# Performance work log

Measured on AMD Instinct MI355X. Metric: run time of the kernel, lower is better.

Reference implementation:

```python
import jax, jax.numpy as jnp
import numpy as np

N0, N1, E, B = 100000, 100000, 800000, 1024
F0, F1 = 93, 43


def _gin(x, src, dst, w, b, n):
    # GINConv(eps=0): h_i = Lin(x_i + sum_{j->i} x_j)
    agg = jax.ops.segment_sum(x[src], dst, num_segments=n)
    return (x + agg) @ w + b


def _pool(x, batch, num_graphs):
    s = jax.ops.segment_sum(x, batch, num_segments=num_graphs)
    cnt = jax.ops.segment_sum(jnp.ones((x.shape[0],), x.dtype), batch, num_segments=num_graphs)
    mean = s / jnp.maximum(cnt, 1.0)[:, None]
    mx = jax.ops.segment_max(x, batch, num_segments=num_graphs)
    return jnp.concatenate([mean, mx], axis=1)


def _pairnorm(x, eps=1e-5):
    x = x - x.mean(axis=0, keepdims=True)
    return x / jnp.sqrt(eps + (x * x).sum(-1).mean())


def _bn(x, gamma, beta, eps=1e-5):
    mu = x.mean(axis=0, keepdims=True)
    var = x.var(axis=0, keepdims=True)
    return (x - mu) / jnp.sqrt(var + eps) * gamma + beta


def _branch(x, ei, batch, n, wc_a, bc_a, wc_b, bc_b, fg_w1, fg_b1, fg_w2, fg_b2, fg_g, fg_bt, ff_w1, ff_b1, ff_w2, ff_b2):
    src, dst = ei[0], ei[1]
    h = jax.nn.relu(_gin(x, src, dst, wc_a, bc_a, n))
    h = jax.nn.relu(_gin(h, src, dst, wc_b, bc_b, n))
    g = _pairnorm(_pool(h, batch, B))
    g = jax.nn.relu(g @ fg_w1 + fg_b1)
    g = _bn(g @ fg_w2 + fg_b2, fg_g, fg_bt)  # [B, 512]
    z = jax.nn.relu(g @ ff_w1 + ff_b1)
    z = jax.nn.sigmoid(z @ ff_w2 + ff_b2)  # [B, 2]
    return z[:, 0], z[:, 1], g


def setup_inputs() -> dict:
    key = jax.random.key(0)
    ks = iter(jax.random.split(key, 40))

    def lin(fan_in, fan_out):
        bnd = 1.0 / np.sqrt(fan_in)
        w = jax.random.uniform(next(ks), (fan_in, fan_out), jnp.float32, -bnd, bnd)
        b = jax.random.uniform(next(ks), (fan_out,), jnp.float32, -bnd, bnd)
        return w, b

    x0 = jax.random.normal(next(ks), (N0, F0), jnp.float32)
    x1 = jax.random.normal(next(ks), (N1, F1), jnp.float32)
    ei0 = jax.random.randint(next(ks), (2, E), 0, N0, jnp.int32)
    ei1 = jax.random.randint(next(ks), (2, E), 0, N1, jnp.int32)
    b0 = jnp.sort(jax.random.randint(next(ks), (N0,), 0, B, jnp.int32))
    b1 = jnp.sort(jax.random.randint(next(ks), (N1,), 0, B, jnp.int32))

    inp = {"x0": x0, "edge_index_0": ei0, "batch_0": b0, "x1": x1, "edge_index_1": ei1, "batch_1": b1}
    inp["w_c1"], inp["b_c1"] = lin(F0, F0)
    inp["w_c2"], inp["b_c2"] = lin(F0, F0 * 10)
    inp["w_c3"], inp["b_c3"] = lin(F1, F1)
    inp["w_c4"], inp["b_c4"] = lin(F1, F1 * 10)
    inp["fg0_w1"], inp["fg0_b1"] = lin(F0 * 10 * 2, 1024)
    inp["fg0_w2"], inp["fg0_b2"] = lin(1024, 512)
    inp["fg0_g"], inp["fg0_bt"] = jnp.ones((512,), jnp.float32), jnp.zeros((512,), jnp.float32)
    inp["fg1_w1"], inp["fg1_b1"] = lin(F1 * 10 * 2, 1024)
    inp["fg1_w2"], inp["fg1_b2"] = lin(1024, 512)
    inp["fg1_g"], inp["fg1_bt"] = jnp.ones((512,), jnp.float32), jnp.zeros((512,), jnp.float32)
    inp["ff0_w1"], inp["ff0_b1"] = lin(512, 256)
    inp["ff0_w2"], inp["ff0_b2"] = lin(256, 2)
    inp["ff1_w1"], inp["ff1_b1"] = lin(512, 256)
    inp["ff1_w2"], inp["ff1_b2"] = lin(256, 2)
    return inp


def reference(x0, edge_index_0, batch_0, x1, edge_index_1, batch_1,
              w_c1, b_c1, w_c2, b_c2, w_c3, b_c3, w_c4, b_c4,
              fg0_w1, fg0_b1, fg0_w2, fg0_b2, fg0_g, fg0_bt,
              fg1_w1, fg1_b1, fg1_w2, fg1_b2, fg1_g, fg1_bt,
              ff0_w1, ff0_b1, ff0_w2, ff0_b2,
              ff1_w1, ff1_b1, ff1_w2, ff1_b2):
    alpha, beta, xg0 = _branch(x0, edge_index_0, batch_0, N0, w_c1, b_c1, w_c2, b_c2,
                               fg0_w1, fg0_b1, fg0_w2, fg0_b2, fg0_g, fg0_bt,
                               ff0_w1, ff0_b1, ff0_w2, ff0_b2)
    alpha1, beta1, xg1 = _branch(x1, edge_index_1, batch_1, N1, w_c3, b_c3, w_c4, b_c4,
                                 fg1_w1, fg1_b1, fg1_w2, fg1_b2, fg1_g, fg1_bt,
                                 ff1_w1, ff1_b1, ff1_w2, ff1_b2)
    return (alpha, beta, xg0, xg1, alpha1, beta1)
```

## Files before the change

kernel.cpp:

```cpp
#include <hip/hip_runtime.h>
#include <hip/hip_bf16.h>
#include <math.h>

#define EDGES 800000
#define NNODES 100000
#define NGRAPH 1024
#define SCAN_B 256

typedef __attribute__((ext_vector_type(8))) short short8v;
typedef __attribute__((ext_vector_type(4))) float float4v;
typedef unsigned short ushort_t;

__device__ inline ushort_t f2bf(float f) {
  __hip_bfloat16 h = __float2bfloat16(f);
  return *reinterpret_cast<ushort_t*>(&h);
}
__device__ inline float bf2f(ushort_t u) {
  return __uint_as_float(((unsigned int)u) << 16);
}

__global__ __launch_bounds__(256) void deg_k(const int* __restrict__ dst,
                                             int* __restrict__ deg, int E) {
  int e = blockIdx.x * 256 + threadIdx.x;
  if (e < E) atomicAdd(&deg[dst[e]], 1);
}

__global__ __launch_bounds__(SCAN_B) void scan_block_k(const int* __restrict__ deg,
                                                       int* __restrict__ scanned,
                                                       int* __restrict__ bsum, int n) {
  __shared__ int tmp[SCAN_B];
  int b = blockIdx.x, t = threadIdx.x, i = b * SCAN_B + t;
  int v = (i < n) ? deg[i] : 0;
  tmp[t] = v;
  __syncthreads();
  for (int off = 1; off < SCAN_B; off <<= 1) {
    int x = (t >= off) ? tmp[t - off] : 0;
    __syncthreads();
    tmp[t] += x;
    __syncthreads();
  }
  if (i < n) scanned[i] = tmp[t] - v;
  if (t == SCAN_B - 1) bsum[b] = tmp[t];
}

__global__ __launch_bounds__(512) void scan_sums_k(int* __restrict__ bsum, int nb) {
  __shared__ int tmp[512];
  int t = threadIdx.x;
  int v = (t < nb) ? bsum[t] : 0;
  tmp[t] = v;
  __syncthreads();
  for (int off = 1; off < 512; off <<= 1) {
    int x = (t >= off) ? tmp[t - off] : 0;
    __syncthreads();
    tmp[t] += x;
    __syncthreads();
  }
  if (t < nb) bsum[t] = tmp[t] - v;
}

__global__ __launch_bounds__(256) void scan_add_k(const int* __restrict__ scanned,
                                                  const int* __restrict__ bsum,
                                                  int* __restrict__ rowstart, int n,
                                                  int total) {
  int i = blockIdx.x * 256 + threadIdx.x;
  if (i < n) rowstart[i] = scanned[i] + bsum[i / SCAN_B];
  if (i == 0) rowstart[n] = total;
}

#define NBMAX 512
__global__ __launch_bounds__(256) void bscatter_k(const int* __restrict__ src,
                                                  const int* __restrict__ dst,
                                                  const int* __restrict__ rowstart,
                                                  int* __restrict__ bcur,
                                                  int2* __restrict__ EB, int E,
                                                  int NB) {
  __shared__ int hist[NBMAX], run[NBMAX], lcur[NBMAX];
  int t = threadIdx.x;
  for (int b = t; b < NB; b += 256) {
    hist[b] = 0;
    lcur[b] = 0;
  }
  __syncthreads();
  int e0 = blockIdx.x * 4096;
  int e1 = min(E, e0 + 4096);
  for (int e = e0 + t; e < e1; e += 256) atomicAdd(&hist[dst[e] >> 8], 1);
  __syncthreads();
  for (int b = t; b < NB; b += 256)
    if (hist[b] > 0) run[b] = atomicAdd(&bcur[b], hist[b]);
  __syncthreads();
  for (int e = e0 + t; e < e1; e += 256) {
    int d = dst[e];
    int b = d >> 8;
    int l = atomicAdd(&lcur[b], 1);
    int pos = rowstart[b << 8] + run[b] + l;
    EB[pos] = make_int2(src[e], d);
  }
}

__global__ __launch_bounds__(256) void fill2_k(const int2* __restrict__ EB,
                                               const int* __restrict__ rowstart,
                                               int* __restrict__ cur,
                                               int* __restrict__ adj, int E) {
  int e = blockIdx.x * 256 + threadIdx.x;
  if (e >= E) return;
  int2 ed = EB[e];
  int p = rowstart[ed.y] + atomicAdd(&cur[ed.y], 1);
  adj[p] = ed.x;
}

__global__ __launch_bounds__(256) void gstart_k(const int* __restrict__ bat,
                                                int* __restrict__ gs, int N, int B) {
  int g = blockIdx.x * 256 + threadIdx.x;
  if (g > B) return;
  if (g == B) {
    gs[B] = N;
    return;
  }
  int lo = 0, hi = N;
  while (lo < hi) {
    int mid = (lo + hi) >> 1;
    if (bat[mid] < g) lo = mid + 1;
    else hi = mid;
  }
  gs[g] = lo;
}

template <int KP>
__global__ __launch_bounds__(256) void tobf16_k(const float* __restrict__ x,
                                                ushort_t* __restrict__ out, int M,
                                                int F) {
  long i = (long)blockIdx.x * 256 + threadIdx.x;
  if (i >= (long)M * KP) return;
  int r = (int)(i / KP), c = (int)(i % KP);
  float v = (c < F) ? x[(long)r * F + c] : 0.f;
  out[i] = f2bf(v);
}

template <int KP>
__global__ __launch_bounds__(256) void gather_k(const ushort_t* __restrict__ X,
                                                const int* __restrict__ rowstart,
                                                const int* __restrict__ adj,
                                                ushort_t* __restrict__ out, int M) {
  constexpr int CH = KP / 8;
  long tid = (long)blockIdx.x * 256 + threadIdx.x;
  if (tid >= (long)M * CH) return;
  int node = (int)(tid / CH), ch = (int)(tid % CH);
  int o = ch * 8;
  float acc[8];
  uint4 self = *(const uint4*)&X[(long)node * KP + o];
  {
    const unsigned int u[4] = {self.x, self.y, self.z, self.w};
#pragma unroll
    for (int i = 0; i < 4; ++i) {
      acc[2 * i] = __uint_as_float((u[i] & 0xFFFFu) << 16);
      acc[2 * i + 1] = __uint_as_float(u[i] & 0xFFFF0000u);
    }
  }
  int rs = rowstart[node], re = rowstart[node + 1];
  for (int e = rs; e < re; ++e) {
    int j = adj[e];
    uint4 v = *(const uint4*)&X[(long)j * KP + o];
    const unsigned int u[4] = {v.x, v.y, v.z, v.w};
#pragma unroll
    for (int i = 0; i < 4; ++i) {
      acc[2 * i] += __uint_as_float((u[i] & 0xFFFFu) << 16);
      acc[2 * i + 1] += __uint_as_float(u[i] & 0xFFFF0000u);
    }
  }
  uint4 r;
  unsigned int* p = &r.x;
#pragma unroll
  for (int i = 0; i < 4; ++i) {
    unsigned int lo = f2bf(acc[2 * i]);
    unsigned int hi = f2bf(acc[2 * i + 1]);
    p[i] = lo | (hi << 16);
  }
  *(uint4*)&out[(long)node * KP + o] = r;
}

__global__ __launch_bounds__(256) void wt_k(const float* __restrict__ W,
                                            ushort_t* __restrict__ WT, int K, int N,
                                            int KP, int Npad) {
  int i = blockIdx.x * 256 + threadIdx.x;
  if (i >= Npad * KP) return;
  int n = i / KP, k = i % KP;
  float v = (k < K && n < N) ? W[(long)k * N + n] : 0.f;
  WT[i] = f2bf(v);
}

template <int KP>
__global__ __launch_bounds__(256) void conv_gemm2_k(
    const ushort_t* __restrict__ A, const ushort_t* __restrict__ WT,
    const float* __restrict__ bias, ushort_t* __restrict__ Cout, int M, int Nc,
    int OW, int NT) {
  constexpr int NKS = KP / 32;
  int tid = threadIdx.x;
  int wid = tid >> 6, lane = tid & 63;
  int lr = lane & 15, q = lane >> 4;
  int lk = q * 8;
  int row0 = blockIdx.x * 64;
  int arow = row0 + wid * 16 + lr;

  short8v a[NKS];
  const ushort_t* ap = A + (long)arow * KP + lk;
#pragma unroll
  for (int ks = 0; ks < NKS; ++ks) a[ks] = *(const short8v*)(ap + ks * 32);

  for (int ct = 0; ct < NT; ++ct) {
    int col0 = ct * 64;
    float4v acc[4];
#pragma unroll
    for (int i = 0; i < 4; ++i) acc[i] = (float4v){0.f, 0.f, 0.f, 0.f};
#pragma unroll
    for (int ks = 0; ks < NKS; ++ks) {
#pragma unroll
      for (int nf = 0; nf < 4; ++nf) {
        short8v b =
            *(const short8v*)&WT[(long)(col0 + nf * 16 + lr) * KP + ks * 32 + lk];
        acc[nf] = __builtin_amdgcn_mfma_f32_16x16x32_bf16(a[ks], b, acc[nf], 0, 0, 0);
      }
    }
#pragma unroll
    for (int nf = 0; nf < 4; ++nf) {
      int gc = col0 + nf * 16 + lr;
      if (gc >= OW) continue;
      float bv = (gc < Nc) ? bias[gc] : 0.f;
#pragma unroll
      for (int i = 0; i < 4; ++i) {
        int gr = row0 + wid * 16 + q * 4 + i;
        if (gr < M) {
          float v = (gc < Nc) ? fmaxf(acc[nf][i] + bv, 0.f) : 0.f;
          Cout[(long)gr * OW + gc] = f2bf(v);
        }
      }
    }
  }
}

template <int KP>
__global__ __launch_bounds__(64) void conv_pool2_k(
    const ushort_t* __restrict__ A, const ushort_t* __restrict__ WT,
    const float* __restrict__ bias, const int* __restrict__ gstart,
    float* __restrict__ pool, int Nc, int NCpool) {
  constexpr int NKS = KP / 32;
  int g = blockIdx.x;
  int col0 = blockIdx.y * 64;
  int rs = gstart[g], re = gstart[g + 1];
  int rows = re - rs;
  int lane = threadIdx.x;
  int lr = lane & 15, q = lane >> 4, lk = q * 8;

  short8v bfr[NKS][4];
  float bv[4];
#pragma unroll
  for (int nf = 0; nf < 4; ++nf) {
    int gc = col0 + nf * 16 + lr;
    bv[nf] = (gc < Nc) ? bias[gc] : 0.f;
#pragma unroll
    for (int ks = 0; ks < NKS; ++ks)
      bfr[ks][nf] = *(const short8v*)&WT[(long)gc * KP + ks * 32 + lk];
  }

  float wsum[4][4] = {}, wmax[4][4] = {};
  int nch = (rows + 15) / 16;
  for (int c = 0; c < nch; ++c) {
    const ushort_t* ap = A + (long)(rs + c * 16 + lr) * KP + lk;
    short8v a[NKS];
#pragma unroll
    for (int ks = 0; ks < NKS; ++ks) a[ks] = *(const short8v*)(ap + ks * 32);
    float4v acc[4];
#pragma unroll
    for (int i = 0; i < 4; ++i) acc[i] = (float4v){0.f, 0.f, 0.f, 0.f};
#pragma unroll
    for (int ks = 0; ks < NKS; ++ks)
#pragma unroll
      for (int nf = 0; nf < 4; ++nf)
        acc[nf] = __builtin_amdgcn_mfma_f32_16x16x32_bf16(a[ks], bfr[ks][nf],
                                                          acc[nf], 0, 0, 0);
    int rbase = c * 16 + q * 4;
#pragma unroll
    for (int i = 0; i < 4; ++i) {
      bool ok = rbase + i < rows;
#pragma unroll
      for (int nf = 0; nf < 4; ++nf) {
        float v = ok ? fmaxf(acc[nf][i] + bv[nf], 0.f) : 0.f;
        wsum[nf][i] += v;
        wmax[nf][i] = fmaxf(wmax[nf][i], v);
      }
    }
  }

  float inv = 1.f / fmaxf((float)rows, 1.f);
#pragma unroll
  for (int nf = 0; nf < 4; ++nf) {
    float s = (wsum[nf][0] + wsum[nf][1]) + (wsum[nf][2] + wsum[nf][3]);
    float m = fmaxf(fmaxf(wmax[nf][0], wmax[nf][1]),
                    fmaxf(wmax[nf][2], wmax[nf][3]));
    s += __shfl_xor(s, 16);
    s += __shfl_xor(s, 32);
    m = fmaxf(m, __shfl_xor(m, 16));
    m = fmaxf(m, __shfl_xor(m, 32));
    int gc = col0 + nf * 16 + lr;
    if (q == 0 && gc < Nc) {
      pool[(long)g * 2 * NCpool + gc] = s * inv;
      pool[(long)g * 2 * NCpool + NCpool + gc] = m;
    }
  }
}

__global__ __launch_bounds__(256) void fc_mfma_k(const ushort_t* __restrict__ A,
                                                 const ushort_t* __restrict__ WT,
                                                 float* __restrict__ PART, int KP,
                                                 int Nc, int Kc) {
  int tid = threadIdx.x;
  int wid = tid >> 6, lane = tid & 63;
  int lr = lane & 15, q = lane >> 4, lk = q * 8;
  int row0 = blockIdx.y * 64, col0 = blockIdx.x * 64;
  int M = gridDim.y * 64;
  int kbeg = blockIdx.z * Kc;
  int arow = row0 + wid * 16 + lr;
  const ushort_t* ap = A + (long)arow * KP + kbeg + lk;
  const ushort_t* wp = WT + (long)col0 * KP + kbeg + lk;

  float4v acc[4];
#pragma unroll
  for (int i = 0; i < 4; ++i) acc[i] = (float4v){0.f, 0.f, 0.f, 0.f};

  for (int k0 = 0; k0 < Kc; k0 += 32) {
    short8v a = *(const short8v*)(ap + k0);
#pragma unroll
    for (int nf = 0; nf < 4; ++nf) {
      short8v b = *(const short8v*)(wp + (long)(nf * 16 + lr) * KP + k0);
      acc[nf] = __builtin_amdgcn_mfma_f32_16x16x32_bf16(a, b, acc[nf], 0, 0, 0);
    }
  }

  float* P = PART + (long)blockIdx.z * M * Nc;
#pragma unroll
  for (int nf = 0; nf < 4; ++nf) {
    int gc = col0 + nf * 16 + lr;
#pragma unroll
    for (int i = 0; i < 4; ++i) {
      int gr = row0 + wid * 16 + q * 4 + i;
      P[(long)gr * Nc + gc] = acc[nf][i];
    }
  }
}

__global__ __launch_bounds__(256) void sk_epi2_k(const float* __restrict__ PART,
                                                 const float* __restrict__ bias,
                                                 float* __restrict__ Cf,
                                                 ushort_t* __restrict__ Cb, int M,
                                                 int Nc, int SK, int relu) {
  long idx = (long)blockIdx.x * 256 + threadIdx.x;
  if (idx >= (long)M * Nc) return;
  int c = (int)(idx % Nc);
  float s = bias[c];
  for (int z = 0; z < SK; ++z) s += PART[(long)z * M * Nc + idx];
  if (relu) s = fmaxf(s, 0.f);
  if (Cf) Cf[idx] = s;
  if (Cb) Cb[idx] = f2bf(s);
}

__global__ __launch_bounds__(256) void colstat_part_k(const float* __restrict__ X,
                                                      float* __restrict__ PS,
                                                      float* __restrict__ ssqtot,
                                                      int Rows, int Cols, int CR) {
  __shared__ float sred[256];
  int c0 = blockIdx.x * 64;
  int chunk = blockIdx.y;
  int t = threadIdx.x;
  int c = c0 + (t & 63);
  int rg = t >> 6;
  int rbeg = chunk * CR, rend = min(Rows, rbeg + CR);
  float s = 0.f, s2 = 0.f;
  if (c < Cols) {
    for (int r = rbeg + rg; r < rend; r += 4) {
      float v = X[(long)r * Cols + c];
      s += v;
      s2 += v * v;
    }
  }
  sred[t] = s;
  __syncthreads();
  if (t < 64 && c0 + t < Cols)
    PS[(long)chunk * Cols + c0 + t] = sred[t] + sred[t + 64] + sred[t + 128] + sred[t + 192];
  for (int off = 32; off > 0; off >>= 1) s2 += __shfl_down(s2, off);
  if ((t & 63) == 0) atomicAdd(ssqtot, s2);
}

__global__ __launch_bounds__(256) void colstat_fin_k(const float* __restrict__ PS,
                                                     float* __restrict__ cm, int Rows,
                                                     int Cols, int nchunk) {
  int c = blockIdx.x * 256 + threadIdx.x;
  if (c >= Cols) return;
  float s = 0.f;
  for (int z = 0; z < nchunk; ++z) s += PS[(long)z * Cols + c];
  cm[c] = s / Rows;
}

__global__ __launch_bounds__(256) void pn_scale_k(const float* __restrict__ cm,
                                                  const float* __restrict__ ssqtot,
                                                  float* __restrict__ scale, int Rows,
                                                  int Cols) {
  __shared__ float red[256];
  int t = threadIdx.x;
  float s = 0.f;
  for (int i = t; i < Cols; i += 256) {
    float v = cm[i];
    s += v * v;
  }
  red[t] = s;
  __syncthreads();
  for (int off = 128; off > 0; off >>= 1) {
    if (t < off) red[t] += red[t + off];
    __syncthreads();
  }
  if (t == 0) {
    float ssq = ssqtot[0] - (float)Rows * red[0];
    scale[0] = 1.f / sqrtf(1e-5f + ssq / Rows);
  }
}

__global__ __launch_bounds__(256) void pn_apply2_k(const float* __restrict__ X,
                                                   const float* __restrict__ cm,
                                                   const float* __restrict__ scale,
                                                   ushort_t* __restrict__ outB,
                                                   int Rows, int Cols, int KP1) {
  long idx = (long)blockIdx.x * 256 + threadIdx.x;
  if (idx >= (long)Rows * KP1) return;
  int r = (int)(idx / KP1), c = (int)(idx % KP1);
  float v = 0.f;
  if (c < Cols) v = (X[(long)r * Cols + c] - cm[c]) * scale[0];
  outB[idx] = f2bf(v);
}

__global__ __launch_bounds__(256) void bn_part_k(const float* __restrict__ X,
                                                 float* __restrict__ PS,
                                                 float* __restrict__ PQ, int Rows,
                                                 int Cols, int CR) {
  __shared__ float s1[256], s2l[256];
  int c0 = blockIdx.x * 64;
  int chunk = blockIdx.y;
  int t = threadIdx.x;
  int c = c0 + (t & 63);
  int rg = t >> 6;
  int rbeg = chunk * CR, rend = min(Rows, rbeg + CR);
  float a = 0.f, b = 0.f;
  if (c < Cols) {
    for (int r = rbeg + rg; r < rend; r += 4) {
      float v = X[(long)r * Cols + c];
      a += v;
      b += v * v;
    }
  }
  s1[t] = a;
  s2l[t] = b;
  __syncthreads();
  if (t < 64 && c0 + t < Cols) {
    PS[(long)chunk * Cols + c0 + t] = s1[t] + s1[t + 64] + s1[t + 128] + s1[t + 192];
    PQ[(long)chunk * Cols + c0 + t] = s2l[t] + s2l[t + 64] + s2l[t + 128] + s2l[t + 192];
  }
}

__global__ __launch_bounds__(256) void bn_fin_k(const float* __restrict__ PS,
                                                const float* __restrict__ PQ,
                                                float* __restrict__ mu,
                                                float* __restrict__ var, int Rows,
                                                int Cols, int nchunk) {
  int c = blockIdx.x * 256 + threadIdx.x;
  if (c >= Cols) return;
  float s = 0.f, q = 0.f;
  for (int z = 0; z < nchunk; ++z) {
    s += PS[(long)z * Cols + c];
    q += PQ[(long)z * Cols + c];
  }
  float m = s / Rows;
  mu[c] = m;
  var[c] = q / Rows - m * m;
}

__global__ void bn_apply2_k(float* __restrict__ X, const float* __restrict__ mu,
                            const float* __restrict__ var, const float* __restrict__ g,
                            const float* __restrict__ b, ushort_t* __restrict__ XB16,
                            int Rows, int Cols) {
  long idx = (long)blockIdx.x * 256 + threadIdx.x;
  if (idx >= (long)Rows * Cols) return;
  int c = (int)(idx % Cols);
  float v = (X[idx] - mu[c]) / sqrtf(var[c] + 1e-5f) * g[c] + b[c];
  X[idx] = v;
  XB16[idx] = f2bf(v);
}

__global__ __launch_bounds__(64) void ff2_k(const ushort_t* __restrict__ Z,
                                            const float* __restrict__ W2,
                                            const float* __restrict__ b2,
                                            float* __restrict__ alpha,
                                            float* __restrict__ beta, int K) {
  int row = blockIdx.x;
  int t = threadIdx.x;
  float s0 = 0.f, s1 = 0.f;
  for (int k = t; k < K; k += 64) {
    float z = bf2f(Z[(long)row * K + k]);
    s0 += z * W2[2 * k];
    s1 += z * W2[2 * k + 1];
  }
  for (int off = 32; off > 0; off >>= 1) {
    s0 += __shfl_down(s0, off);
    s1 += __shfl_down(s1, off);
  }
  if (t == 0) {
    alpha[row] = 1.f / (1.f + expf(-(s0 + b2[0])));
    beta[row] = 1.f / (1.f + expf(-(s1 + b2[1])));
  }
}

template <int KP>
static void run_branch(const float* x, const int* ei, const int* bat,
                       const float* wc1, const float* bc1, const float* wc2,
                       const float* bc2, const float* fgw1, const float* fgb1,
                       const float* fgw2, const float* fgb2, const float* fgg,
                       const float* fgbt, const float* ffw1, const float* ffb1,
                       const float* ffw2, const float* ffb2, int N, int F,
                       float* out_alpha, float* out_beta, float* out_xg,
                       ushort_t* XB, ushort_t* XA, ushort_t* H, ushort_t* WT,
                       int* deg, int* scanned, int* rowstart, int* cur, int* bsum,
                       int* bcur, int* adj, int* GS, float* POOL, float* CM,
                       float* MU, float* VAR, float* SSQ, float* PSUM, float* PSQ,
                       ushort_t* POOLB, ushort_t* WTF1, ushort_t* WTF2,
                       ushort_t* WTFF, ushort_t* G1B, ushort_t* XGB, ushort_t* Z1B,
                       float* PART, hipStream_t stream) {
  const int NC = F * 10;
  const int Bn = NGRAPH;
  const int* src = ei;
  const int* dst = ei + EDGES;
  const int MB = (N + 63) / 64;
  const int Mpad = MB * 64;
  const int nb = (N + SCAN_B - 1) / SCAN_B;
  const int NB = (N + 255) >> 8;

  int2* EB = (int2*)XB;
  hipMemsetAsync(deg, 0, (size_t)N * 4, stream);
  hipMemsetAsync(cur, 0, (size_t)N * 4, stream);
  hipMemsetAsync(bcur, 0, NBMAX * 4, stream);
  deg_k<<<(EDGES + 255) / 256, 256, 0, stream>>>(dst, deg, EDGES);
  scan_block_k<<<nb, SCAN_B, 0, stream>>>(deg, scanned, bsum, N);
  scan_sums_k<<<1, 512, 0, stream>>>(bsum, nb);
  scan_add_k<<<nb, 256, 0, stream>>>(scanned, bsum, rowstart, N, EDGES);
  bscatter_k<<<(EDGES + 4095) / 4096, 256, 0, stream>>>(src, dst, rowstart, bcur, EB, EDGES, NB);
  fill2_k<<<(EDGES + 255) / 256, 256, 0, stream>>>(EB, rowstart, cur, adj, EDGES);
  gstart_k<<<(NGRAPH + 256) / 256, 256, 0, stream>>>(bat, GS, N, NGRAPH);

  constexpr int CH = KP / 8;
  if (Mpad > N)
    hipMemsetAsync(XA + (size_t)N * KP, 0, (size_t)(Mpad - N) * KP * 2, stream);
  tobf16_k<KP><<<(int)(((long)N * KP + 255) / 256), 256, 0, stream>>>(x, XB, N, F);
  gather_k<KP><<<(int)(((long)N * CH + 255) / 256), 256, 0, stream>>>(XB, rowstart, adj, XA, N);
  wt_k<<<(((F + 63) / 64) * 64 * KP + 255) / 256, 256, 0, stream>>>(
      wc1, WT, F, F, KP, ((F + 63) / 64) * 64);
  conv_gemm2_k<KP><<<MB, 256, 0, stream>>>(XA, WT, bc1, H, N, F, KP, (KP + 63) / 64);
  gather_k<KP><<<(int)(((long)N * CH + 255) / 256), 256, 0, stream>>>(H, rowstart, adj, XA, N);
  int Npad2 = ((NC + 63) / 64) * 64;
  wt_k<<<(Npad2 * KP + 255) / 256, 256, 0, stream>>>(wc2, WT, F, NC, KP, Npad2);
  conv_pool2_k<KP><<<dim3(NGRAPH, Npad2 / 64), 64, 0, stream>>>(XA, WT, bc2, GS, POOL, NC, NC);

  int Cols = 2 * NC;
  const int NCH = 16, CR = NGRAPH / NCH;
  hipMemsetAsync(SSQ, 0, 8, stream);
  colstat_part_k<<<dim3((Cols + 63) / 64, NCH), 256, 0, stream>>>(POOL, PSUM, SSQ, Bn, Cols, CR);
  colstat_fin_k<<<(Cols + 255) / 256, 256, 0, stream>>>(PSUM, CM, Bn, Cols, NCH);
  pn_scale_k<<<1, 256, 0, stream>>>(CM, SSQ, SSQ + 1, Bn, Cols);

  int KP1 = ((Cols + 127) / 128) * 128;
  pn_apply2_k<<<(int)(((long)Bn * KP1 + 255) / 256), 256, 0, stream>>>(
      POOL, CM, SSQ + 1, POOLB, Bn, Cols, KP1);
  wt_k<<<(1024 * KP1 + 255) / 256, 256, 0, stream>>>(fgw1, WTF1, Cols, 1024, KP1, 1024);
  fc_mfma_k<<<dim3(16, 16, 4), 256, 0, stream>>>(POOLB, WTF1, PART, KP1, 1024, KP1 / 4);
  sk_epi2_k<<<(Bn * 1024 + 255) / 256, 256, 0, stream>>>(PART, fgb1, nullptr, G1B, Bn, 1024, 4, 1);
  wt_k<<<(512 * 1024 + 255) / 256, 256, 0, stream>>>(fgw2, WTF2, 1024, 512, 1024, 512);
  fc_mfma_k<<<dim3(8, 16, 4), 256, 0, stream>>>(G1B, WTF2, PART, 1024, 512, 256);
  sk_epi2_k<<<(Bn * 512 + 255) / 256, 256, 0, stream>>>(PART, fgb2, out_xg, nullptr, Bn, 512, 4, 0);
  bn_part_k<<<dim3(8, 8), 256, 0, stream>>>(out_xg, PSUM, PSQ, Bn, 512, 128);
  bn_fin_k<<<2, 256, 0, stream>>>(PSUM, PSQ, MU, VAR, Bn, 512, 8);
  bn_apply2_k<<<(Bn * 512 + 255) / 256, 256, 0, stream>>>(out_xg, MU, VAR, fgg, fgbt, XGB, Bn, 512);
  wt_k<<<(256 * 512 + 255) / 256, 256, 0, stream>>>(ffw1, WTFF, 512, 256, 512, 256);
  fc_mfma_k<<<dim3(4, 16, 8), 256, 0, stream>>>(XGB, WTFF, PART, 512, 256, 64);
  sk_epi2_k<<<(Bn * 256 + 255) / 256, 256, 0, stream>>>(PART, ffb1, nullptr, Z1B, Bn, 256, 8, 1);
  ff2_k<<<Bn, 64, 0, stream>>>(Z1B, ffw2, ffb2, out_alpha, out_beta, 256);
}

extern "C" void kernel_launch(void* const* d_in, const int* in_sizes, int n_in,
                              void* d_out, int out_size, void* d_ws, size_t ws_size,
                              hipStream_t stream) {
  if (n_in < 34) return;
  const float* x0 = (const float*)d_in[0];
  const int* ei0 = (const int*)d_in[1];
  const int* b0 = (const int*)d_in[2];
  const float* x1 = (const float*)d_in[3];
  const int* ei1 = (const int*)d_in[4];
  const int* b1 = (const int*)d_in[5];
  const float* w_c1 = (const float*)d_in[6];
  const float* b_c1 = (const float*)d_in[7];
  const float* w_c2 = (const float*)d_in[8];
  const float* b_c2 = (const float*)d_in[9];
  const float* w_c3 = (const float*)d_in[10];
  const float* b_c3 = (const float*)d_in[11];
  const float* w_c4 = (const float*)d_in[12];
  const float* b_c4 = (const float*)d_in[13];
  const float* fg0_w1 = (const float*)d_in[14];
  const float* fg0_b1 = (const float*)d_in[15];
  const float* fg0_w2 = (const float*)d_in[16];
  const float* fg0_b2 = (const float*)d_in[17];
  const float* fg0_g = (const float*)d_in[18];
  const float* fg0_bt = (const float*)d_in[19];
  const float* fg1_w1 = (const float*)d_in[20];
  const float* fg1_b1 = (const float*)d_in[21];
  const float* fg1_w2 = (const float*)d_in[22];
  const float* fg1_b2 = (const float*)d_in[23];
  const float* fg1_g = (const float*)d_in[24];
  const float* fg1_bt = (const float*)d_in[25];
  const float* ff0_w1 = (const float*)d_in[26];
  const float* ff0_b1 = (const float*)d_in[27];
  const float* ff0_w2 = (const float*)d_in[28];
  const float* ff0_b2 = (const float*)d_in[29];
  const float* ff1_w1 = (const float*)d_in[30];
  const float* ff1_b1 = (const float*)d_in[31];
  const float* ff1_w2 = (const float*)d_in[32];
  const float* ff1_b2 = (const float*)d_in[33];

  float* out = (float*)d_out;
  float* alpha = out;
  float* beta = out + 1024;
  float* xg0 = out + 2048;
  float* xg1 = out + 2048 + 1024 * 512;
  float* alpha1 = out + 2048 + 2 * 1024 * 512;
  float* beta1 = alpha1 + 1024;

  char* w = (char*)d_ws;
  auto alloc = [&](size_t bytes) -> void* {
    void* p = (void*)w;
    w += ((bytes + 255) / 256) * 256;
    return p;
  };
  const int Mpad = ((NNODES + 63) / 64) * 64;
  ushort_t* XB = (ushort_t*)alloc((size_t)Mpad * 96 * 2);
  ushort_t* XA = (ushort_t*)alloc((size_t)Mpad * 96 * 2);
  ushort_t* H = (ushort_t*)alloc((size_t)Mpad * 96 * 2);
  ushort_t* WT = (ushort_t*)alloc((size_t)960 * 96 * 2);
  int* deg = (int*)alloc((size_t)(NNODES + 1) * 4);
  int* scanned = (int*)alloc((size_t)(NNODES + 1) * 4);
  int* rowstart = (int*)alloc((size_t)(NNODES + 1) * 4);
  int* cur = (int*)alloc((size_t)NNODES * 4);
  int* bsum = (int*)alloc(512 * 4);
  int* bcur = (int*)alloc(NBMAX * 4);
  int* adj = (int*)alloc((size_t)EDGES * 4);
  int* GS = (int*)alloc((size_t)(NGRAPH + 1) * 4);
  float* POOL = (float*)alloc((size_t)NGRAPH * 1860 * 4);
  float* CM = (float*)alloc(1860 * 4);
  float* MU = (float*)alloc(512 * 4);
  float* VAR = (float*)alloc(512 * 4);
  float* SSQ = (float*)alloc(256);
  float* PSUM = (float*)alloc((size_t)16 * 1920 * 4);
  float* PSQ = (float*)alloc((size_t)8 * 512 * 4);
  ushort_t* POOLB = (ushort_t*)alloc((size_t)NGRAPH * 1920 * 2);
  ushort_t* WTF1 = (ushort_t*)alloc((size_t)1024 * 1920 * 2);
  ushort_t* WTF2 = (ushort_t*)alloc((size_t)512 * 1024 * 2);
  ushort_t* WTFF = (ushort_t*)alloc((size_t)256 * 512 * 2);
  ushort_t* G1B = (ushort_t*)alloc((size_t)NGRAPH * 1024 * 2);
  ushort_t* XGB = (ushort_t*)alloc((size_t)NGRAPH * 512 * 2);
  ushort_t* Z1B = (ushort_t*)alloc((size_t)NGRAPH * 256 * 2);
  if ((size_t)(w - (char*)d_ws) > ws_size) return;

  float* PART = (float*)XB;

  run_branch<96>(x0, ei0, b0, w_c1, b_c1, w_c2, b_c2, fg0_w1, fg0_b1, fg0_w2,
                 fg0_b2, fg0_g, fg0_bt, ff0_w1, ff0_b1, ff0_w2, ff0_b2, NNODES,
                 93, alpha, beta, xg0, XB, XA, H, WT, deg, scanned, rowstart,
                 cur, bsum, bcur, adj, GS, POOL, CM, MU, VAR, SSQ, PSUM, PSQ,
                 POOLB, WTF1, WTF2, WTFF, G1B, XGB, Z1B, PART, stream);
  run_branch<64>(x1, ei1, b1, w_c3, b_c3, w_c4, b_c4, fg1_w1, fg1_b1, fg1_w2,
                 fg1_b2, fg1_g, fg1_bt, ff1_w1, ff1_b1, ff1_w2, ff1_b2, NNODES,
                 43, alpha1, beta1, xg1, XB, XA, H, WT, deg, scanned, rowstart,
                 cur, bsum, bcur, adj, GS, POOL, CM, MU, VAR, SSQ, PSUM, PSQ,
                 POOLB, WTF1, WTF2, WTFF, G1B, XGB, Z1B, PART, stream);
}
```

Measured before the change: 720.1 us.

## Build CSR via two-level bucket sort instead of per-node degree scan

Replaces the per-node degree atomics, three-kernel multi-block scan and global-atomic CSR fill with a bucket-level count and scan over 256-node buckets. A per-bucket kernel then builds node row starts and the adjacency list using shared-memory counting. This removes several launches, two memsets and the global atomics on per-node counters. It adds a shared-memory serial-ish per-bucket pass, whose load depends on bucket size, about 2k edges each.

Result: faster. 629.2 us (-12.6%).

```diff
diff --git a/kernel.cpp b/kernel.cpp
--- a/kernel.cpp
+++ b/kernel.cpp
@@ -5,7 +5,6 @@
 #define EDGES 800000
 #define NNODES 100000
 #define NGRAPH 1024
-#define SCAN_B 256
 
 typedef __attribute__((ext_vector_type(8))) short short8v;
 typedef __attribute__((ext_vector_type(4))) float float4v;
@@ -19,34 +18,28 @@
   return __uint_as_float(((unsigned int)u) << 16);
 }
 
-__global__ __launch_bounds__(256) void deg_k(const int* __restrict__ dst,
-                                             int* __restrict__ deg, int E) {
-  int e = blockIdx.x * 256 + threadIdx.x;
-  if (e < E) atomicAdd(&deg[dst[e]], 1);
-}
-
-__global__ __launch_bounds__(SCAN_B) void scan_block_k(const int* __restrict__ deg,
-                                                       int* __restrict__ scanned,
-                                                       int* __restrict__ bsum, int n) {
-  __shared__ int tmp[SCAN_B];
-  int b = blockIdx.x, t = threadIdx.x, i = b * SCAN_B + t;
-  int v = (i < n) ? deg[i] : 0;
-  tmp[t] = v;
-  __syncthreads();
-  for (int off = 1; off < SCAN_B; off <<= 1) {
-    int x = (t >= off) ? tmp[t - off] : 0;
-    __syncthreads();
-    tmp[t] += x;
-    __syncthreads();
-  }
-  if (i < n) scanned[i] = tmp[t] - v;
-  if (t == SCAN_B - 1) bsum[b] = tmp[t];
-}
-
-__global__ __launch_bounds__(512) void scan_sums_k(int* __restrict__ bsum, int nb) {
+#define NBMAX 512
+
+__global__ __launch_bounds__(256) void bcount_k(const int* __restrict__ dst,
+                                                int* __restrict__ bcnt, int E,
+                                                int NB) {
+  __shared__ int hist[NBMAX];
+  int t = threadIdx.x;
+  for (int b = t; b < NB; b += 256) hist[b] = 0;
+  __syncthreads();
+  int e0 = blockIdx.x * 4096;
+  int e1 = min(E, e0 + 4096);
+  for (int e = e0 + t; e < e1; e += 256) atomicAdd(&hist[dst[e] >> 8], 1);
+  __syncthreads();
+  for (int b = t; b < NB; b += 256)
+    if (hist[b] > 0) atomicAdd(&bcnt[b], hist[b]);
+}
+
+__global__ __launch_bounds__(512) void bscan_k(const int* __restrict__ bcnt,
+                                               int* __restrict__ boff, int NB) {
   __shared__ int tmp[512];
   int t = threadIdx.x;
-  int v = (t < nb) ? bsum[t] : 0;
+  int v = (t < NB) ? bcnt[t] : 0;
   tmp[t] = v;
   __syncthreads();
   for (int off = 1; off < 512; off <<= 1) {
@@ -55,22 +48,13 @@
     tmp[t] += x;
     __syncthreads();
   }
-  if (t < nb) bsum[t] = tmp[t] - v;
-}
-
-__global__ __launch_bounds__(256) void scan_add_k(const int* __restrict__ scanned,
-                                                  const int* __restrict__ bsum,
-                                                  int* __restrict__ rowstart, int n,
-                                                  int total) {
-  int i = blockIdx.x * 256 + threadIdx.x;
-  if (i < n) rowstart[i] = scanned[i] + bsum[i / SCAN_B];
-  if (i == 0) rowstart[n] = total;
-}
-
-#define NBMAX 512
+  if (t < NB) boff[t] = tmp[t] - v;
+  if (t == NB - 1) boff[NB] = tmp[t];
+}
+
 __global__ __launch_bounds__(256) void bscatter_k(const int* __restrict__ src,
                                                   const int* __restrict__ dst,
-                                                  const int* __restrict__ rowstart,
+                                                  const int* __restrict__ boff,
                                                   int* __restrict__ bcur,
                                                   int2* __restrict__ EB, int E,
                                                   int NB) {
@@ -92,20 +76,43 @@
     int d = dst[e];
     int b = d >> 8;
     int l = atomicAdd(&lcur[b], 1);
-    int pos = rowstart[b << 8] + run[b] + l;
+    int pos = boff[b] + run[b] + l;
     EB[pos] = make_int2(src[e], d);
   }
 }
 
-__global__ __launch_bounds__(256) void fill2_k(const int2* __restrict__ EB,
-                                               const int* __restrict__ rowstart,
-                                               int* __restrict__ cur,
-                                               int* __restrict__ adj, int E) {
-  int e = blockIdx.x * 256 + threadIdx.x;
-  if (e >= E) return;
-  int2 ed = EB[e];
-  int p = rowstart[ed.y] + atomicAdd(&cur[ed.y], 1);
-  adj[p] = ed.x;
+__global__ __launch_bounds__(256) void bucket_csr_k(const int2* __restrict__ EB,
+                                                    const int* __restrict__ boff,
+                                                    int* __restrict__ rowstart,
+                                                    int* __restrict__ adj, int N,
+                                                    int NB, int E) {
+  __shared__ int cnt[256], pfx[256], lcur[256];
+  int b = blockIdx.x, t = threadIdx.x;
+  int e0 = boff[b], e1 = boff[b + 1];
+  cnt[t] = 0;
+  __syncthreads();
+  for (int e = e0 + t; e < e1; e += 256) atomicAdd(&cnt[EB[e].y & 255], 1);
+  __syncthreads();
+  int v = cnt[t];
+  pfx[t] = v;
+  __syncthreads();
+  for (int off = 1; off < 256; off <<= 1) {
+    int x = (t >= off) ? pfx[t - off] : 0;
+    __syncthreads();
+    pfx[t] += x;
+    __syncthreads();
+  }
+  int node = (b << 8) + t;
+  if (node < N) rowstart[node] = e0 + pfx[t] - v;
+  if (b == NB - 1 && t == 0) rowstart[N] = E;
+  lcur[t] = 0;
+  __syncthreads();
+  for (int e = e0 + t; e < e1; e += 256) {
+    int2 ed = EB[e];
+    int ln = ed.y & 255;
+    int l = atomicAdd(&lcur[ln], 1);
+    adj[e0 + pfx[ln] - cnt[ln] + l] = ed.x;
+  }
 }
 
 __global__ __launch_bounds__(256) void gstart_k(const int* __restrict__ bat,
@@ -524,31 +531,27 @@
                        const float* ffw2, const float* ffb2, int N, int F,
                        float* out_alpha, float* out_beta, float* out_xg,
                        ushort_t* XB, ushort_t* XA, ushort_t* H, ushort_t* WT,
-                       int* deg, int* scanned, int* rowstart, int* cur, int* bsum,
-                       int* bcur, int* adj, int* GS, float* POOL, float* CM,
-                       float* MU, float* VAR, float* SSQ, float* PSUM, float* PSQ,
-                       ushort_t* POOLB, ushort_t* WTF1, ushort_t* WTF2,
-                       ushort_t* WTFF, ushort_t* G1B, ushort_t* XGB, ushort_t* Z1B,
-                       float* PART, hipStream_t stream) {
+                       int* rowstart, int* BC, int* boff, int* adj, int* GS,
+                       float* POOL, float* CM, float* MU, float* VAR, float* SSQ,
+                       float* PSUM, float* PSQ, ushort_t* POOLB, ushort_t* WTF1,
+                       ushort_t* WTF2, ushort_t* WTFF, ushort_t* G1B, ushort_t* XGB,
+                       ushort_t* Z1B, float* PART, hipStream_t stream) {
   const int NC = F * 10;
   const int Bn = NGRAPH;
   const int* src = ei;
   const int* dst = ei + EDGES;
   const int MB = (N + 63) / 64;
   const int Mpad = MB * 64;
-  const int nb = (N + SCAN_B - 1) / SCAN_B;
   const int NB = (N + 255) >> 8;
 
   int2* EB = (int2*)XB;
-  hipMemsetAsync(deg, 0, (size_t)N * 4, stream);
-  hipMemsetAsync(cur, 0, (size_t)N * 4, stream);
-  hipMemsetAsync(bcur, 0, NBMAX * 4, stream);
-  deg_k<<<(EDGES + 255) / 256, 256, 0, stream>>>(dst, deg, EDGES);
-  scan_block_k<<<nb, SCAN_B, 0, stream>>>(deg, scanned, bsum, N);
-  scan_sums_k<<<1, 512, 0, stream>>>(bsum, nb);
-  scan_add_k<<<nb, 256, 0, stream>>>(scanned, bsum, rowstart, N, EDGES);
-  bscatter_k<<<(EDGES + 4095) / 4096, 256, 0, stream>>>(src, dst, rowstart, bcur, EB, EDGES, NB);
-  fill2_k<<<(EDGES + 255) / 256, 256, 0, stream>>>(EB, rowstart, cur, adj, EDGES);
+  int* bcnt = BC;
+  int* bcur = BC + NBMAX;
+  hipMemsetAsync(BC, 0, 2 * NBMAX * 4, stream);
+  bcount_k<<<(EDGES + 4095) / 4096, 256, 0, stream>>>(dst, bcnt, EDGES, NB);
+  bscan_k<<<1, 512, 0, stream>>>(bcnt, boff, NB);
+  bscatter_k<<<(EDGES + 4095) / 4096, 256, 0, stream>>>(src, dst, boff, bcur, EB, EDGES, NB);
+  bucket_csr_k<<<NB, 256, 0, stream>>>(EB, boff, rowstart, adj, N, NB, EDGES);
   gstart_k<<<(NGRAPH + 256) / 256, 256, 0, stream>>>(bat, GS, N, NGRAPH);
 
   constexpr int CH = KP / 8;
@@ -647,12 +650,9 @@
   ushort_t* XA = (ushort_t*)alloc((size_t)Mpad * 96 * 2);
   ushort_t* H = (ushort_t*)alloc((size_t)Mpad * 96 * 2);
   ushort_t* WT = (ushort_t*)alloc((size_t)960 * 96 * 2);
-  int* deg = (int*)alloc((size_t)(NNODES + 1) * 4);
-  int* scanned = (int*)alloc((size_t)(NNODES + 1) * 4);
   int* rowstart = (int*)alloc((size_t)(NNODES + 1) * 4);
-  int* cur = (int*)alloc((size_t)NNODES * 4);
-  int* bsum = (int*)alloc(512 * 4);
-  int* bcur = (int*)alloc(NBMAX * 4);
+  int* BC = (int*)alloc(2 * NBMAX * 4);
+  int* boff = (int*)alloc((NBMAX + 1) * 4);
   int* adj = (int*)alloc((size_t)EDGES * 4);
   int* GS = (int*)alloc((size_t)(NGRAPH + 1) * 4);
   float* POOL = (float*)alloc((size_t)NGRAPH * 1860 * 4);
@@ -675,12 +675,12 @@
 
   run_branch<96>(x0, ei0, b0, w_c1, b_c1, w_c2, b_c2, fg0_w1, fg0_b1, fg0_w2,
                  fg0_b2, fg0_g, fg0_bt, ff0_w1, ff0_b1, ff0_w2, ff0_b2, NNODES,
-                 93, alpha, beta, xg0, XB, XA, H, WT, deg, scanned, rowstart,
-                 cur, bsum, bcur, adj, GS, POOL, CM, MU, VAR, SSQ, PSUM, PSQ,
-                 POOLB, WTF1, WTF2, WTFF, G1B, XGB, Z1B, PART, stream);
+                 93, alpha, beta, xg0, XB, XA, H, WT, rowstart, BC, boff, adj, GS,
+                 POOL, CM, MU, VAR, SSQ, PSUM, PSQ, POOLB, WTF1, WTF2, WTFF, G1B,
+                 XGB, Z1B, PART, stream);
   run_branch<64>(x1, ei1, b1, w_c3, b_c3, w_c4, b_c4, fg1_w1, fg1_b1, fg1_w2,
                  fg1_b2, fg1_g, fg1_bt, ff1_w1, ff1_b1, ff1_w2, ff1_b2, NNODES,
-                 43, alpha1, beta1, xg1, XB, XA, H, WT, deg, scanned, rowstart,
-                 cur, bsum, bcur, adj, GS, POOL, CM, MU, VAR, SSQ, PSUM, PSQ,
-                 POOLB, WTF1, WTF2, WTFF, G1B, XGB, Z1B, PART, stream);
-}
+                 43, alpha1, beta1, xg1, XB, XA, H, WT, rowstart, BC, boff, adj,
+                 GS, POOL, CM, MU, VAR, SSQ, PSUM, PSQ, POOLB, WTF1, WTF2, WTFF,
+                 G1B, XGB, Z1B, PART, stream);
+}
```
